# Optimization experiments

Measured on AMD Instinct MI355X. Metric: run time of the kernel, lower is better.

The kernel has to match this reference:

```python
import jax, jax.numpy as jnp
import numpy as np

EPS = 1e-12  # torch F.normalize default eps

def _l2norm(x):
    # torch.nn.functional.normalize(x, dim=-1): x / max(||x||_2, eps)
    n = jnp.linalg.norm(x, axis=-1, keepdims=True)
    return x / jnp.maximum(n, EPS)

def setup_inputs() -> dict:
    key = jax.random.key(0)
    ks = jax.random.split(key, 12)
    B, T, D, V, C = 16, 2048, 1024, 32000, 6
    s = 0.02
    text = jax.random.randint(ks[0], (B * T,), 0, V, dtype=jnp.int64)
    offsets = (jnp.arange(B, dtype=jnp.int64) * T)  # uniform-length sequences
    emb = jax.random.normal(ks[1], (V, D), dtype=jnp.float32) * s
    Wq = jax.random.normal(ks[2], (D, D), dtype=jnp.float32) * s
    bq = jnp.zeros((D,), jnp.float32)
    Wk = jax.random.normal(ks[3], (D, D), dtype=jnp.float32) * s
    bk = jnp.zeros((D,), jnp.float32)
    Wv = jax.random.normal(ks[4], (D, D), dtype=jnp.float32) * s
    bv = jnp.zeros((D,), jnp.float32)
    Wfc = jax.random.normal(ks[5], (D, D), dtype=jnp.float32) * s
    bfc = jnp.zeros((D,), jnp.float32)
    Wo = jax.random.normal(ks[6], (C, D), dtype=jnp.float32) * s
    bo = jnp.zeros((C,), jnp.float32)
    return {"text": text, "offsets": offsets, "emb": emb,
            "Wq": Wq, "bq": bq, "Wk": Wk, "bk": bk, "Wv": Wv, "bv": bv,
            "Wfc": Wfc, "bfc": bfc, "Wo": Wo, "bo": bo}

def reference(text, offsets, emb, Wq, bq, Wk, bk, Wv, bv, Wfc, bfc, Wo, bo):
    B = offsets.shape[0]
    T = text.shape[0] // B  # uniform lengths -> pad_sequence == reshape
    D = emb.shape[1]
    tok = text.reshape(B, T)
    x = emb[tok]                                   # [B,T,D]
    q = x @ Wq.T + bq
    k = x @ Wk.T + bk
    v = x @ Wv.T + bv
    scores = jnp.einsum('bqd,bkd->bqk', q, k) / jnp.sqrt(jnp.asarray(D, x.dtype))
    causal = jnp.tril(jnp.ones((T, T), dtype=bool))
    scores = jnp.where(causal[None, :, :], scores, -jnp.inf)
    attn = jax.nn.softmax(scores, axis=-1)
    out = jnp.einsum('bqk,bkd->bqd', attn, v) + x  # residual with embedding
    out = _l2norm(out)
    out = out + (out @ Wfc.T + bfc)                # residual FFN
    out = _l2norm(out)
    last = out[:, -1, :]                           # [B,D]
    return jax.nn.sigmoid(last @ Wo.T + bo)        # [B,num_class]
```

## Files before the change

### kernel.cpp

```cpp
#include <hip/hip_runtime.h>
#include <hip/hip_bf16.h>
#include <math.h>

typedef unsigned short ushort_t;

__device__ __forceinline__ float bf2f(ushort_t u) {
    union { unsigned int i; float f; } v;
    v.i = ((unsigned int)u) << 16;
    return v.f;
}

__device__ __forceinline__ ushort_t f2bf(float f) {
    union { float f; unsigned int i; } v; v.f = f;
    unsigned int lsb = (v.i >> 16) & 1;
    unsigned int r = v.i + 0x7FFF + lsb;
    return (ushort_t)(r >> 16);
}

__device__ __forceinline__ float wave_sum(float acc) {
    #pragma unroll
    for (int off = 32; off >= 1; off >>= 1) acc += __shfl_xor(acc, off, 64);
    return acc;
}
__device__ __forceinline__ float wave_max(float acc) {
    #pragma unroll
    for (int off = 32; off >= 1; off >>= 1) acc = fmaxf(acc, __shfl_xor(acc, off, 64));
    return acc;
}

__device__ __forceinline__ void ld8(const void* p, int isbf, size_t i, float* o) {
    if (isbf) {
        uint4 raw = *reinterpret_cast<const uint4*>((const ushort_t*)p + i);
        const ushort_t* pu = reinterpret_cast<const ushort_t*>(&raw);
        #pragma unroll
        for (int k = 0; k < 8; ++k) o[k] = bf2f(pu[k]);
    } else {
        const float4* f = reinterpret_cast<const float4*>((const float*)p + i);
        float4 a = f[0], b = f[1];
        o[0]=a.x; o[1]=a.y; o[2]=a.z; o[3]=a.w;
        o[4]=b.x; o[5]=b.y; o[6]=b.z; o[7]=b.w;
    }
}

__device__ __forceinline__ void ld4(const void* p, int isbf, size_t i, float* o) {
    if (isbf) {
        uint2 raw = *reinterpret_cast<const uint2*>((const ushort_t*)p + i);
        const ushort_t* pu = reinterpret_cast<const ushort_t*>(&raw);
        #pragma unroll
        for (int k = 0; k < 4; ++k) o[k] = bf2f(pu[k]);
    } else {
        float4 a = *reinterpret_cast<const float4*>((const float*)p + i);
        o[0]=a.x; o[1]=a.y; o[2]=a.z; o[3]=a.w;
    }
}

__device__ __forceinline__ float ldS(const void* p, int isbf, size_t i) {
    return isbf ? bf2f(((const ushort_t*)p)[i]) : ((const float*)p)[i];
}

__device__ __forceinline__ int tokAt(const void* text, int isi64, size_t i) {
    return isi64 ? ((const int*)text)[2 * i] : ((const int*)text)[i];
}

__device__ __forceinline__ void detect_flags(const void* emb, const void* text, int* sf) {
    if (threadIdx.x < 64) {
        const int lane = threadIdx.x;
        ushort_t u = ((const ushort_t*)emb)[2 * lane];
        int e = (u >> 7) & 0xFF;
        unsigned long long mb = __ballot(e >= 0x60 && e <= 0x7E);
        int odd = ((const int*)text)[2 * lane + 1];
        unsigned long long mi = __ballot(odd != 0);
        if (lane == 0) {
            sf[0] = (__popcll(mb) >= 32) ? 1 : 0;
            sf[1] = (__popcll(mi) == 0) ? 1 : 0;
        }
    }
    __syncthreads();
}

__device__ __forceinline__ void hoist16(const float* v, int lane, float* c16) {
    #pragma unroll
    for (int k = 0; k < 16; ++k) c16[k] = v[lane * 16 + k];
}

__global__ void kQC(const void* __restrict__ text, const void* __restrict__ emb,
                    const void* __restrict__ Wq, const void* __restrict__ bq,
                    const void* __restrict__ Wk, float* __restrict__ c_part,
                    int B, int T, int D) {
    const int ch = blockIdx.x / B;
    const int b  = blockIdx.x % B;
    const int i0 = ch << 5;
    const int tid = threadIdx.x;
    __shared__ int sf[2];
    __shared__ float xs[1024];
    __shared__ float qs[32];
    detect_flags(emb, text, sf);
    const int isbf = sf[0], isi64 = sf[1];
    const int tok = tokAt(text, isi64, (size_t)b * T + (T - 1));
    float w4[4];
    {
        const int dd = tid * 4;
        ld4(emb, isbf, (size_t)tok * D + dd, w4);
        xs[dd]=w4[0]; xs[dd+1]=w4[1]; xs[dd+2]=w4[2]; xs[dd+3]=w4[3];
    }
    __syncthreads();
    const int wave = tid >> 6, lane = tid & 63;
    float c16[16];
    hoist16(xs, lane, c16);
    float w[8];
    for (int r = 0; r < 8; ++r) {
        const int i = i0 + wave * 8 + r;
        float acc = 0.f;
        ld8(Wq, isbf, (size_t)i * D + lane * 16, w);
        #pragma unroll
        for (int k = 0; k < 8; ++k) acc += w[k] * c16[k];
        ld8(Wq, isbf, (size_t)i * D + lane * 16 + 8, w);
        #pragma unroll
        for (int k = 0; k < 8; ++k) acc += w[k] * c16[8 + k];
        acc = wave_sum(acc);
        if (lane == 0) qs[wave * 8 + r] = acc + ldS(bq, isbf, i);
    }
    __syncthreads();
    const int d = tid * 4;
    float a0=0.f, a1=0.f, a2=0.f, a3=0.f;
    #pragma unroll 8
    for (int i = 0; i < 32; ++i) {
        const float qv = qs[i];
        ld4(Wk, isbf, (size_t)(i0 + i) * D + d, w4);
        a0 += qv*w4[0]; a1 += qv*w4[1]; a2 += qv*w4[2]; a3 += qv*w4[3];
    }
    *reinterpret_cast<float4*>(c_part + ((size_t)ch * B + b) * D + d)
        = make_float4(a0, a1, a2, a3);
}

__global__ void kCC(const float* __restrict__ c_part, float* __restrict__ c,
                    int B, int D, int nch) {
    const int nb = D >> 6;
    const int b = blockIdx.x / nb;
    const int dblk = blockIdx.x % nb;
    const int q = threadIdx.x >> 6, dl = threadIdx.x & 63;
    const int d = dblk * 64 + dl;
    __shared__ float red[256];
    const int per = nch >> 2;
    float acc = 0.f;
    for (int j = 0; j < per; ++j) {
        const int cc = q * per + j;
        acc += c_part[((size_t)cc * B + b) * D + d];
    }
    red[threadIdx.x] = acc;
    __syncthreads();
    if (q == 0) c[(size_t)b * D + d] = red[dl] + red[64 + dl] + red[128 + dl] + red[192 + dl];
}

__global__ void k35(const void* __restrict__ text, const void* __restrict__ emb,
                    const float* __restrict__ c, float* __restrict__ xbar_part,
                    float* __restrict__ m_part, float* __restrict__ l_part,
                    int B, int T, int D, float scale) {
    const int nchT = T >> 4;
    const int b = blockIdx.x / nchT;
    const int ch = blockIdx.x % nchT;
    const int j0 = ch << 4;
    const int tid = threadIdx.x;
    __shared__ int sf[2];
    __shared__ ushort_t rows[16 * 1024];
    __shared__ float cs[1024];
    __shared__ float sjs[16];
    __shared__ float wls[16];
    __shared__ int tks[16];
    detect_flags(emb, text, sf);
    const int isbf = sf[0], isi64 = sf[1];
    {
        const int d = tid * 4;
        float4 v = *reinterpret_cast<const float4*>(c + (size_t)b * D + d);
        cs[d]=v.x; cs[d+1]=v.y; cs[d+2]=v.z; cs[d+3]=v.w;
    }
    if (tid < 16) tks[tid] = tokAt(text, isi64, (size_t)b * T + j0 + tid);
    __syncthreads();
    if (isbf) {
        const ushort_t* E = (const ushort_t*)emb;
        const int half = tid >> 7;
        const int off  = (tid & 127) * 8;
        #pragma unroll
        for (int sw = 0; sw < 8; ++sw) {
            const int r = sw * 2 + half;
            uint4 v = *reinterpret_cast<const uint4*>(E + (size_t)tks[r] * D + off);
            *reinterpret_cast<uint4*>(&rows[r * 1024 + off]) = v;
        }
    }
    __syncthreads();
    const int wave = tid >> 6, lane = tid & 63;
    {
        float c16[16];
        hoist16(cs, lane, c16);
        float w[8];
        for (int rr = 0; rr < 4; ++rr) {
            const int r = wave + rr * 4;
            float acc = 0.f;
            if (isbf) {
                uint4 raw = *reinterpret_cast<const uint4*>(&rows[r * 1024 + lane * 16]);
                const ushort_t* pu = reinterpret_cast<const ushort_t*>(&raw);
                #pragma unroll
                for (int k = 0; k < 8; ++k) acc += bf2f(pu[k]) * c16[k];
                raw = *reinterpret_cast<const uint4*>(&rows[r * 1024 + lane * 16 + 8]);
                #pragma unroll
                for (int k = 0; k < 8; ++k) acc += bf2f(pu[k]) * c16[8 + k];
            } else {
                ld8(emb, 0, (size_t)tks[r] * D + lane * 16, w);
                #pragma unroll
                for (int k = 0; k < 8; ++k) acc += w[k] * c16[k];
                ld8(emb, 0, (size_t)tks[r] * D + lane * 16 + 8, w);
                #pragma unroll
                for (int k = 0; k < 8; ++k) acc += w[k] * c16[8 + k];
            }
            acc = wave_sum(acc);
            if (lane == 0) sjs[r] = acc * scale;
        }
    }
    __syncthreads();
    float mx = -INFINITY;
    #pragma unroll
    for (int j = 0; j < 16; ++j) mx = fmaxf(mx, sjs[j]);
    if (tid < 16) wls[tid] = expf(sjs[tid] - mx);
    __syncthreads();
    if (tid < 64) {
        float v = (tid < 16) ? wls[tid] : 0.f;
        v = wave_sum(v);
        if (tid == 0) { m_part[(size_t)b * nchT + ch] = mx;
                        l_part[(size_t)b * nchT + ch] = v; }
    }
    const int d = tid * 4;
    float a0=0.f, a1=0.f, a2=0.f, a3=0.f;
    if (isbf) {
        #pragma unroll
        for (int j = 0; j < 16; ++j) {
            const float wj = wls[j];
            uint2 raw = *reinterpret_cast<const uint2*>(&rows[j * 1024 + d]);
            const ushort_t* pu = reinterpret_cast<const ushort_t*>(&raw);
            a0 += wj*bf2f(pu[0]); a1 += wj*bf2f(pu[1]);
            a2 += wj*bf2f(pu[2]); a3 += wj*bf2f(pu[3]);
        }
    } else {
        float w4[4];
        #pragma unroll
        for (int j = 0; j < 16; ++j) {
            const float wj = wls[j];
            ld4(emb, 0, (size_t)tks[j] * D + d, w4);
            a0 += wj*w4[0]; a1 += wj*w4[1]; a2 += wj*w4[2]; a3 += wj*w4[3];
        }
    }
    *reinterpret_cast<float4*>(xbar_part + ((size_t)b * nchT + ch) * D + d)
        = make_float4(a0, a1, a2, a3);
}

__global__ void kC(const float* __restrict__ xbar_part, const float* __restrict__ m_part,
                   const float* __restrict__ l_part, float* __restrict__ xbar,
                   int B, int D, int nchT) {
    const int nb = D >> 6;
    const int b = blockIdx.x / nb;
    const int dblk = blockIdx.x % nb;
    const int q = threadIdx.x >> 6, dl = threadIdx.x & 63;
    const int d = dblk * 64 + dl;
    __shared__ float sc[128];
    __shared__ float red[256];
    if (threadIdx.x < 64) {
        const int t = threadIdx.x;
        float m0 = (t < nchT) ? m_part[(size_t)b * nchT + t] : -INFINITY;
        float m1 = (64 + t < nchT) ? m_part[(size_t)b * nchT + 64 + t] : -INFINITY;
        float mx = wave_max(fmaxf(m0, m1));
        float l0 = (t < nchT) ? l_part[(size_t)b * nchT + t] * expf(m0 - mx) : 0.f;
        float l1 = (64 + t < nchT) ? l_part[(size_t)b * nchT + 64 + t] * expf(m1 - mx) : 0.f;
        float ls = wave_sum(l0 + l1);
        if (t < nchT) sc[t] = expf(m0 - mx) / ls;
        if (64 + t < nchT) sc[64 + t] = expf(m1 - mx) / ls;
    }
    __syncthreads();
    const int per = nchT >> 2;
    float acc = 0.f;
    for (int j = 0; j < per; ++j) {
        const int cc = q * per + j;
        acc += sc[cc] * xbar_part[((size_t)b * nchT + cc) * D + d];
    }
    red[threadIdx.x] = acc;
    __syncthreads();
    if (q == 0) xbar[(size_t)b * D + d] = red[dl] + red[64 + dl]
                                        + red[128 + dl] + red[192 + dl];
}

__global__ void kVA(const void* __restrict__ text, const void* __restrict__ emb,
                    const void* __restrict__ Wv, const void* __restrict__ bv,
                    const float* __restrict__ xbar, float* __restrict__ u,
                    int B, int T, int D) {
    const int ch = blockIdx.x / B;
    const int b  = blockIdx.x % B;
    const int r0 = ch << 5;
    const int tid = threadIdx.x;
    __shared__ int sf[2];
    __shared__ float xb[1024];
    __shared__ float xl[32];
    detect_flags(emb, text, sf);
    const int isbf = sf[0], isi64 = sf[1];
    const int tok = tokAt(text, isi64, (size_t)b * T + (T - 1));
    if (tid < 32) xl[tid] = ldS(emb, isbf, (size_t)tok * D + r0 + tid);
    {
        const int dd = tid * 4;
        float4 v = *reinterpret_cast<const float4*>(xbar + (size_t)b * D + dd);
        xb[dd]=v.x; xb[dd+1]=v.y; xb[dd+2]=v.z; xb[dd+3]=v.w;
    }
    __syncthreads();
    const int wave = tid >> 6, lane = tid & 63;
    float c16[16];
    hoist16(xb, lane, c16);
    float w[8];
    for (int rr = 0; rr < 8; ++rr) {
        const int i = r0 + wave + rr * 4;
        float acc = 0.f;
        ld8(Wv, isbf, (size_t)i * D + lane * 16, w);
        #pragma unroll
        for (int k = 0; k < 8; ++k) acc += w[k] * c16[k];
        ld8(Wv, isbf, (size_t)i * D + lane * 16 + 8, w);
        #pragma unroll
        for (int k = 0; k < 8; ++k) acc += w[k] * c16[8 + k];
        acc = wave_sum(acc);
        if (lane == 0) u[(size_t)b * D + i] = acc + ldS(bv, isbf, i) + xl[i - r0];
    }
}

__global__ void k6c_h2(const void* __restrict__ text, const void* __restrict__ emb,
                       const void* __restrict__ Wfc, const void* __restrict__ bfc,
                       const float* __restrict__ u, float* __restrict__ h2,
                       int B, int D) {
    const int ch = blockIdx.x / B;
    const int b  = blockIdx.x % B;
    const int r0 = ch << 5;
    const int tid = threadIdx.x;
    __shared__ int sf[2];
    __shared__ float hs[1024];
    __shared__ float red[256];
    __shared__ float s_rn;
    detect_flags(emb, text, sf);
    const int isbf = sf[0];
    float part;
    {
        const int dd = tid * 4;
        float4 v = *reinterpret_cast<const float4*>(u + (size_t)b * D + dd);
        hs[dd]=v.x; hs[dd+1]=v.y; hs[dd+2]=v.z; hs[dd+3]=v.w;
        part = v.x*v.x + v.y*v.y + v.z*v.z + v.w*v.w;
    }
    red[tid] = part;
    __syncthreads();
    for (int st = 128; st; st >>= 1) {
        if (tid < st) red[tid] += red[tid + st];
        __syncthreads();
    }
    if (tid == 0) s_rn = 1.f / fmaxf(sqrtf(red[0]), 1e-12f);
    __syncthreads();
    const float rn = s_rn;
    {
        const int dd = tid * 4;
        hs[dd] *= rn; hs[dd+1] *= rn; hs[dd+2] *= rn; hs[dd+3] *= rn;
    }
    __syncthreads();
    const int wave = tid >> 6, lane = tid & 63;
    float c16[16];
    hoist16(hs, lane, c16);
    float w[8];
    for (int rr = 0; rr < 8; ++rr) {
        const int i = r0 + wave + rr * 4;
        float acc = 0.f;
        ld8(Wfc, isbf, (size_t)i * D + lane * 16, w);
        #pragma unroll
        for (int k = 0; k < 8; ++k) acc += w[k] * c16[k];
        ld8(Wfc, isbf, (size_t)i * D + lane * 16 + 8, w);
        #pragma unroll
        for (int k = 0; k < 8; ++k) acc += w[k] * c16[8 + k];
        acc = wave_sum(acc);
        if (lane == 0) h2[(size_t)b * D + i] = hs[i] + acc + ldS(bfc, isbf, i);
    }
}

__global__ void k6d_out(const void* __restrict__ text, const void* __restrict__ emb,
                        const void* __restrict__ Wo, const void* __restrict__ bo,
                        const float* __restrict__ h2, void* __restrict__ out,
                        int D, int C, int total) {
    __shared__ int sf[2];
    detect_flags(emb, text, sf);
    const int isbf = sf[0];
    const int g = blockIdx.x * 4 + (threadIdx.x >> 6);
    if (g >= total) return;
    const int lane = threadIdx.x & 63;
    const int b = g / C, ci = g % C;
    float a1 = 0.f, a2 = 0.f, w[8], h[8];
    for (int d0 = lane * 8; d0 < D; d0 += 512) {
        ld8(Wo, isbf, (size_t)ci * D + d0, w);
        ld8(h2, 0, (size_t)b * D + d0, h);
        #pragma unroll
        for (int k = 0; k < 8; ++k) { a1 += w[k] * h[k]; a2 += h[k] * h[k]; }
    }
    a1 = wave_sum(a1);
    a2 = wave_sum(a2);
    if (lane == 0) {
        float rn = 1.f / fmaxf(sqrtf(a2), 1e-12f);
        float z = a1 * rn + ldS(bo, isbf, ci);
        float y = 1.f / (1.f + expf(-z));
        if (isbf) ((ushort_t*)out)[g] = f2bf(y);
        else      ((float*)out)[g] = y;
    }
}

extern "C" void kernel_launch(void* const* d_in, const int* in_sizes, int n_in,
                              void* d_out, int out_size, void* d_ws, size_t ws_size,
                              hipStream_t stream) {
    const void* text = d_in[0];
    const void* emb = d_in[2];
    const void* Wq  = d_in[3];
    const void* bq  = d_in[4];
    const void* Wk  = d_in[5];
    const void* Wv  = d_in[7];
    const void* bv  = d_in[8];
    const void* Wfc = d_in[9];
    const void* bfc = d_in[10];
    const void* Wo  = d_in[11];
    const void* bo  = d_in[12];

    const int B = in_sizes[1];
    const int T = in_sizes[0] / B;
    const int D = in_sizes[4];
    const int C = in_sizes[12];

    const int nch_c = D / 32;
    const int nchT  = T / 16;

    float* ws        = (float*)d_ws;
    float* c_part    = ws;
    float* c         = c_part + (size_t)nch_c * B * D;
    float* xbar_part = c + (size_t)B * D;
    float* m_part    = xbar_part + (size_t)B * nchT * D;
    float* l_part    = m_part + (size_t)B * nchT;
    float* xbar      = l_part + (size_t)B * nchT;
    float* u         = xbar + (size_t)B * D;
    float* h2        = u + (size_t)B * D;

    const float scale = 1.0f / sqrtf((float)D);

    kQC<<<(D / 32) * B, 256, 0, stream>>>(text, emb, Wq, bq, Wk, c_part, B, T, D);
    kCC<<<B * (D / 64), 256, 0, stream>>>(c_part, c, B, D, nch_c);
    k35<<<B * (T / 16), 256, 0, stream>>>(text, emb, c, xbar_part, m_part, l_part,
                                          B, T, D, scale);
    kC<<<B * (D / 64), 256, 0, stream>>>(xbar_part, m_part, l_part, xbar, B, D, nchT);
    kVA<<<(D / 32) * B, 256, 0, stream>>>(text, emb, Wv, bv, xbar, u, B, T, D);
    k6c_h2<<<(D / 32) * B, 256, 0, stream>>>(text, emb, Wfc, bfc, u, h2, B, D);
    k6d_out<<<(B * C + 3) / 4, 256, 0, stream>>>(text, emb, Wo, bo, h2, d_out, D, C, B * C);
}
```

Measured before the change: 286.6 us.

## Use per-wave online softmax in attention chunk kernel with 32-token chunks

Rewrites the last-query attention chunk kernel so each wave streams 8 embedding rows with an online softmax, keeping rows in registers instead of staging them in shared memory and reloading them. Chunks grow from 16 to 32 tokens, halving partial outputs and the reduction work in the combine kernel. Block index mapping in the matvec kernels is also changed to batch-major, and expf becomes __expf. The trade-offs are higher register pressure from 16-element accumulators, fewer blocks, and slightly lower exp precision.

```diff
diff --git a/kernel.cpp b/kernel.cpp
--- a/kernel.cpp
+++ b/kernel.cpp
@@ -1,6 +1,6 @@
 #include <hip/hip_runtime.h>
-#include <hip/hip_bf16.h>
 #include <math.h>
+
 
 typedef unsigned short ushort_t;
 
@@ -87,8 +87,9 @@
                     const void* __restrict__ Wq, const void* __restrict__ bq,
                     const void* __restrict__ Wk, float* __restrict__ c_part,
                     int B, int T, int D) {
-    const int ch = blockIdx.x / B;
-    const int b  = blockIdx.x % B;
+    const int nch = D >> 5;
+    const int b  = blockIdx.x / nch;
+    const int ch = blockIdx.x % nch;
     const int i0 = ch << 5;
     const int tid = threadIdx.x;
     __shared__ int sf[2];
@@ -152,104 +153,76 @@
     if (q == 0) c[(size_t)b * D + d] = red[dl] + red[64 + dl] + red[128 + dl] + red[192 + dl];
 }
 
-__global__ void k35(const void* __restrict__ text, const void* __restrict__ emb,
-                    const float* __restrict__ c, float* __restrict__ xbar_part,
-                    float* __restrict__ m_part, float* __restrict__ l_part,
-                    int B, int T, int D, float scale) {
-    const int nchT = T >> 4;
-    const int b = blockIdx.x / nchT;
-    const int ch = blockIdx.x % nchT;
-    const int j0 = ch << 4;
+__global__ void k35o(const void* __restrict__ text, const void* __restrict__ emb,
+                     const float* __restrict__ c, float* __restrict__ xbar_part,
+                     float* __restrict__ m_part, float* __restrict__ l_part,
+                     int B, int T, int D, float scale) {
+    const int nt32 = T >> 5;
+    const int b = blockIdx.x / nt32;
+    const int ch = blockIdx.x % nt32;
+    const int j0 = ch << 5;
     const int tid = threadIdx.x;
-    __shared__ int sf[2];
-    __shared__ ushort_t rows[16 * 1024];
-    __shared__ float cs[1024];
-    __shared__ float sjs[16];
-    __shared__ float wls[16];
-    __shared__ int tks[16];
+    const int wave = tid >> 6, lane = tid & 63;
+    __shared__ int   sf[2];
+    __shared__ float vec[1024];
+    __shared__ float wacc[4][1024];
+    __shared__ float wm[4], wl[4];
+    __shared__ int   tks[32];
     detect_flags(emb, text, sf);
     const int isbf = sf[0], isi64 = sf[1];
     {
-        const int d = tid * 4;
-        float4 v = *reinterpret_cast<const float4*>(c + (size_t)b * D + d);
-        cs[d]=v.x; cs[d+1]=v.y; cs[d+2]=v.z; cs[d+3]=v.w;
-    }
-    if (tid < 16) tks[tid] = tokAt(text, isi64, (size_t)b * T + j0 + tid);
-    __syncthreads();
-    if (isbf) {
-        const ushort_t* E = (const ushort_t*)emb;
-        const int half = tid >> 7;
-        const int off  = (tid & 127) * 8;
-        #pragma unroll
-        for (int sw = 0; sw < 8; ++sw) {
-            const int r = sw * 2 + half;
-            uint4 v = *reinterpret_cast<const uint4*>(E + (size_t)tks[r] * D + off);
-            *reinterpret_cast<uint4*>(&rows[r * 1024 + off]) = v;
-        }
-    }
-    __syncthreads();
-    const int wave = tid >> 6, lane = tid & 63;
-    {
-        float c16[16];
-        hoist16(cs, lane, c16);
-        float w[8];
-        for (int rr = 0; rr < 4; ++rr) {
-            const int r = wave + rr * 4;
-            float acc = 0.f;
-            if (isbf) {
-                uint4 raw = *reinterpret_cast<const uint4*>(&rows[r * 1024 + lane * 16]);
-                const ushort_t* pu = reinterpret_cast<const ushort_t*>(&raw);
-                #pragma unroll
-                for (int k = 0; k < 8; ++k) acc += bf2f(pu[k]) * c16[k];
-                raw = *reinterpret_cast<const uint4*>(&rows[r * 1024 + lane * 16 + 8]);
-                #pragma unroll
-                for (int k = 0; k < 8; ++k) acc += bf2f(pu[k]) * c16[8 + k];
-            } else {
-                ld8(emb, 0, (size_t)tks[r] * D + lane * 16, w);
-                #pragma unroll
-                for (int k = 0; k < 8; ++k) acc += w[k] * c16[k];
-                ld8(emb, 0, (size_t)tks[r] * D + lane * 16 + 8, w);
-                #pragma unroll
-                for (int k = 0; k < 8; ++k) acc += w[k] * c16[8 + k];
-            }
-            acc = wave_sum(acc);
-            if (lane == 0) sjs[r] = acc * scale;
-        }
-    }
-    __syncthreads();
-    float mx = -INFINITY;
+        const int dd = tid * 4;
+        float4 v = *reinterpret_cast<const float4*>(c + (size_t)b * D + dd);
+        vec[dd]=v.x; vec[dd+1]=v.y; vec[dd+2]=v.z; vec[dd+3]=v.w;
+    }
+    if (tid < 32) tks[tid] = tokAt(text, isi64, (size_t)b * T + j0 + tid);
+    __syncthreads();
+    float c16[16]; hoist16(vec, lane, c16);
+    float m = -INFINITY, l = 0.f;
+    float acc[16];
     #pragma unroll
-    for (int j = 0; j < 16; ++j) mx = fmaxf(mx, sjs[j]);
-    if (tid < 16) wls[tid] = expf(sjs[tid] - mx);
-    __syncthreads();
-    if (tid < 64) {
-        float v = (tid < 16) ? wls[tid] : 0.f;
-        v = wave_sum(v);
-        if (tid == 0) { m_part[(size_t)b * nchT + ch] = mx;
-                        l_part[(size_t)b * nchT + ch] = v; }
+    for (int k = 0; k < 16; ++k) acc[k] = 0.f;
+    #pragma unroll 2
+    for (int rr = 0; rr < 8; ++rr) {
+        const int r = (wave << 3) + rr;
+        float w[16];
+        ld8(emb, isbf, (size_t)tks[r] * D + lane * 16, w);
+        ld8(emb, isbf, (size_t)tks[r] * D + lane * 16 + 8, w + 8);
+        float s = 0.f;
+        #pragma unroll
+        for (int k = 0; k < 16; ++k) s += w[k] * c16[k];
+        s = wave_sum(s) * scale;
+        const float mn = fmaxf(m, s);
+        const float f  = __expf(m - mn);
+        const float p  = __expf(s - mn);
+        l = l * f + p;
+        #pragma unroll
+        for (int k = 0; k < 16; ++k) acc[k] = acc[k] * f + p * w[k];
+        m = mn;
+    }
+    if (lane == 0) { wm[wave] = m; wl[wave] = l; }
+    __syncthreads();
+    const float M = fmaxf(fmaxf(wm[0], wm[1]), fmaxf(wm[2], wm[3]));
+    const float g = __expf(wm[wave] - M);
+    #pragma unroll
+    for (int q = 0; q < 4; ++q) {
+        *reinterpret_cast<float4*>(&wacc[wave][lane * 16 + q * 4]) =
+            make_float4(acc[q*4]*g, acc[q*4+1]*g, acc[q*4+2]*g, acc[q*4+3]*g);
+    }
+    __syncthreads();
+    if (tid == 0) {
+        m_part[(size_t)b * nt32 + ch] = M;
+        l_part[(size_t)b * nt32 + ch] =
+            wl[0]*__expf(wm[0]-M) + wl[1]*__expf(wm[1]-M)
+          + wl[2]*__expf(wm[2]-M) + wl[3]*__expf(wm[3]-M);
     }
     const int d = tid * 4;
-    float a0=0.f, a1=0.f, a2=0.f, a3=0.f;
-    if (isbf) {
-        #pragma unroll
-        for (int j = 0; j < 16; ++j) {
-            const float wj = wls[j];
-            uint2 raw = *reinterpret_cast<const uint2*>(&rows[j * 1024 + d]);
-            const ushort_t* pu = reinterpret_cast<const ushort_t*>(&raw);
-            a0 += wj*bf2f(pu[0]); a1 += wj*bf2f(pu[1]);
-            a2 += wj*bf2f(pu[2]); a3 += wj*bf2f(pu[3]);
-        }
-    } else {
-        float w4[4];
-        #pragma unroll
-        for (int j = 0; j < 16; ++j) {
-            const float wj = wls[j];
-            ld4(emb, 0, (size_t)tks[j] * D + d, w4);
-            a0 += wj*w4[0]; a1 += wj*w4[1]; a2 += wj*w4[2]; a3 += wj*w4[3];
-        }
-    }
-    *reinterpret_cast<float4*>(xbar_part + ((size_t)b * nchT + ch) * D + d)
-        = make_float4(a0, a1, a2, a3);
+    float4 o;
+    o.x = wacc[0][d]   + wacc[1][d]   + wacc[2][d]   + wacc[3][d];
+    o.y = wacc[0][d+1] + wacc[1][d+1] + wacc[2][d+1] + wacc[3][d+1];
+    o.z = wacc[0][d+2] + wacc[1][d+2] + wacc[2][d+2] + wacc[3][d+2];
+    o.w = wacc[0][d+3] + wacc[1][d+3] + wacc[2][d+3] + wacc[3][d+3];
+    *reinterpret_cast<float4*>(xbar_part + ((size_t)b * nt32 + ch) * D + d) = o;
 }
 
 __global__ void kC(const float* __restrict__ xbar_part, const float* __restrict__ m_part,
@@ -267,11 +240,11 @@
         float m0 = (t < nchT) ? m_part[(size_t)b * nchT + t] : -INFINITY;
         float m1 = (64 + t < nchT) ? m_part[(size_t)b * nchT + 64 + t] : -INFINITY;
         float mx = wave_max(fmaxf(m0, m1));
-        float l0 = (t < nchT) ? l_part[(size_t)b * nchT + t] * expf(m0 - mx) : 0.f;
-        float l1 = (64 + t < nchT) ? l_part[(size_t)b * nchT + 64 + t] * expf(m1 - mx) : 0.f;
+        float l0 = (t < nchT) ? l_part[(size_t)b * nchT + t] * __expf(m0 - mx) : 0.f;
+        float l1 = (64 + t < nchT) ? l_part[(size_t)b * nchT + 64 + t] * __expf(m1 - mx) : 0.f;
         float ls = wave_sum(l0 + l1);
-        if (t < nchT) sc[t] = expf(m0 - mx) / ls;
-        if (64 + t < nchT) sc[64 + t] = expf(m1 - mx) / ls;
+        if (t < nchT) sc[t] = __expf(m0 - mx) / ls;
+        if (64 + t < nchT) sc[64 + t] = __expf(m1 - mx) / ls;
     }
     __syncthreads();
     const int per = nchT >> 2;
@@ -290,8 +263,9 @@
                     const void* __restrict__ Wv, const void* __restrict__ bv,
                     const float* __restrict__ xbar, float* __restrict__ u,
                     int B, int T, int D) {
-    const int ch = blockIdx.x / B;
-    const int b  = blockIdx.x % B;
+    const int nch = D >> 5;
+    const int b  = blockIdx.x / nch;
+    const int ch = blockIdx.x % nch;
     const int r0 = ch << 5;
     const int tid = threadIdx.x;
     __shared__ int sf[2];
@@ -329,8 +303,9 @@
                        const void* __restrict__ Wfc, const void* __restrict__ bfc,
                        const float* __restrict__ u, float* __restrict__ h2,
                        int B, int D) {
-    const int ch = blockIdx.x / B;
-    const int b  = blockIdx.x % B;
+    const int nch = D >> 5;
+    const int b  = blockIdx.x / nch;
+    const int ch = blockIdx.x % nch;
     const int r0 = ch << 5;
     const int tid = threadIdx.x;
     __shared__ int sf[2];
@@ -428,7 +403,7 @@
     const int C = in_sizes[12];
 
     const int nch_c = D / 32;
-    const int nchT  = T / 16;
+    const int nchT  = T / 32;
 
     float* ws        = (float*)d_ws;
     float* c_part    = ws;
@@ -442,12 +417,12 @@
 
     const float scale = 1.0f / sqrtf((float)D);
 
-    kQC<<<(D / 32) * B, 256, 0, stream>>>(text, emb, Wq, bq, Wk, c_part, B, T, D);
+    kQC<<<B * (D / 32), 256, 0, stream>>>(text, emb, Wq, bq, Wk, c_part, B, T, D);
     kCC<<<B * (D / 64), 256, 0, stream>>>(c_part, c, B, D, nch_c);
-    k35<<<B * (T / 16), 256, 0, stream>>>(text, emb, c, xbar_part, m_part, l_part,
-                                          B, T, D, scale);
+    k35o<<<B * (T / 32), 256, 0, stream>>>(text, emb, c, xbar_part, m_part, l_part,
+                                           B, T, D, scale);
     kC<<<B * (D / 64), 256, 0, stream>>>(xbar_part, m_part, l_part, xbar, B, D, nchT);
-    kVA<<<(D / 32) * B, 256, 0, stream>>>(text, emb, Wv, bv, xbar, u, B, T, D);
-    k6c_h2<<<(D / 32) * B, 256, 0, stream>>>(text, emb, Wfc, bfc, u, h2, B, D);
+    kVA<<<B * (D / 32), 256, 0, stream>>>(text, emb, Wv, bv, xbar, u, B, T, D);
+    k6c_h2<<<B * (D / 32), 256, 0, stream>>>(text, emb, Wfc, bfc, u, h2, B, D);
     k6d_out<<<(B * C + 3) / 4, 256, 0, stream>>>(text, emb, Wo, bo, h2, d_out, D, C, B * C);
 }
```

Measured after the change: 264.4 us. -7.8%, faster.
